# Kernel tuning notes

Measured on AMD Instinct MI355X. Metric: run time of the kernel, lower is better.

The kernel has to match this reference:

```python
import jax, jax.numpy as jnp
import numpy as np

N_NODES = 50000
NEG_SLOPE = 0.2  # PyG GATConv default
EPS = 1e-16      # PyG softmax denominator epsilon


def gat_conv(x, W, att_src, att_dst, bias, src, dst, heads, out_ch):
    # x: [N, F_in]; W: [F_in, heads*out_ch]; att_*: [heads, out_ch]
    N = x.shape[0]
    h = (x @ W).reshape(N, heads, out_ch)              # [N,H,C]
    a_src = jnp.sum(h * att_src, axis=-1)              # [N,H]
    a_dst = jnp.sum(h * att_dst, axis=-1)              # [N,H]
    alpha = a_src[src] + a_dst[dst]                    # [E,H]
    alpha = jnp.where(alpha > 0, alpha, NEG_SLOPE * alpha)  # leaky_relu
    amax = jax.ops.segment_max(alpha, dst, num_segments=N)  # [N,H]
    amax = jnp.where(jnp.isfinite(amax), amax, 0.0)
    ex = jnp.exp(alpha - amax[dst])                    # [E,H]
    denom = jax.ops.segment_sum(ex, dst, num_segments=N)    # [N,H]
    coef = ex / (denom[dst] + EPS)                     # [E,H]
    msg = h[src] * coef[:, :, None]                    # [E,H,C]
    out = jax.ops.segment_sum(msg, dst, num_segments=N)     # [N,H,C]
    return out.reshape(N, heads * out_ch) + bias


def setup_inputs() -> dict:
    key = jax.random.key(0)
    ks = jax.random.split(key, 11)
    T, N, F = 8, N_NODES, 64
    E = 1_600_000
    x = jax.random.normal(ks[0], (T, N, F), dtype=jnp.float32)
    edge_index = jax.random.randint(ks[1], (2, E), 0, N, dtype=jnp.int64)
    s = 0.1
    return {
        "x": x,
        "edge_index": edge_index,
        "W1": jax.random.normal(ks[2], (F, 64), jnp.float32) * s,
        "att_src1": jax.random.normal(ks[3], (8, 8), jnp.float32) * s,
        "att_dst1": jax.random.normal(ks[4], (8, 8), jnp.float32) * s,
        "bias1": jax.random.normal(ks[5], (64,), jnp.float32) * s,
        "W2": jax.random.normal(ks[6], (64, F), jnp.float32) * s,
        "att_src2": jax.random.normal(ks[7], (1, F), jnp.float32) * s,
        "att_dst2": jax.random.normal(ks[8], (1, F), jnp.float32) * s,
        "bias2": jax.random.normal(ks[9], (F,), jnp.float32) * s,
    }


def reference(x, edge_index, W1, att_src1, att_dst1, bias1, W2, att_src2, att_dst2, bias2):
    N = x.shape[1]
    # PyG GATConv adds self-loops by default
    loops = jnp.arange(N, dtype=edge_index.dtype)
    src = jnp.concatenate([edge_index[0], loops])
    dst = jnp.concatenate([edge_index[1], loops])

    def step(xt):  # xt: [N, F] ; dropout is identity in eval mode
        y = jax.nn.elu(gat_conv(xt, W1, att_src1, att_dst1, bias1, src, dst, 8, 8))
        y = gat_conv(y, W2, att_src2, att_dst2, bias2, src, dst, 1, xt.shape[-1])
        return jax.nn.log_softmax(y, axis=-1)

    return jax.vmap(step)(x)  # [T, N, F]
```

## Files before the change

### kernel.cpp

```cpp
#include <hip/hip_runtime.h>
#include <hip/hip_bf16.h>
#include <math.h>


typedef __hip_bfloat16 bf16;

__device__ __forceinline__ float bf2f(unsigned short u) {
    return __uint_as_float(((unsigned int)u) << 16);
}


__global__ __launch_bounds__(256) void count_edges_kernel(const int* __restrict__ dsts,
                                                          int* cnt, int E) {
    int i = blockIdx.x * 256 + threadIdx.x;
    if (i < E) atomicAdd(&cnt[dsts[i]], 1);
}

__global__ __launch_bounds__(1024) void scan_kernel(const int* __restrict__ cnt,
                                                    int* row, int* cur, int N) {
    __shared__ int ls[1024];
    int t = threadIdx.x;
    int chunk = (N + 1023) / 1024;
    int b = t * chunk;
    int sum = 0;
    for (int i = 0; i < chunk; ++i) {
        int idx = b + i;
        if (idx < N) sum += cnt[idx] + 1;
    }
    ls[t] = sum;
    __syncthreads();
    for (int off = 1; off < 1024; off <<= 1) {
        int v = (t >= off) ? ls[t - off] : 0;
        __syncthreads();
        ls[t] += v;
        __syncthreads();
    }
    int run = (t == 0) ? 0 : ls[t - 1];
    for (int i = 0; i < chunk; ++i) {
        int idx = b + i;
        if (idx < N) {
            int c = cnt[idx] + 1;
            row[idx] = run;
            cur[idx] = run;
            run += c;
        }
    }
    if (t == 1023) row[N] = ls[1023];
}

__global__ __launch_bounds__(256) void fill_csr_kernel(const int* __restrict__ srcs,
                                                       const int* __restrict__ dsts,
                                                       int* cur, int* esrc, int E, int N) {
    int i = blockIdx.x * 256 + threadIdx.x;
    if (i >= E + N) return;
    int s, d;
    if (i < E) { s = srcs[i]; d = dsts[i]; }
    else       { s = i - E;   d = s; }
    int pos = atomicAdd(&cur[d], 1);
    esrc[pos] = s;
}


__device__ __forceinline__ float4 ld4(const float* p) { return *(const float4*)p; }
__device__ __forceinline__ float4 ld4(const bf16* p) {
    ushort4 u = *(const ushort4*)p;
    float4 r;
    r.x = bf2f(u.x); r.y = bf2f(u.y); r.z = bf2f(u.z); r.w = bf2f(u.w);
    return r;
}


template <typename TIN, int H, int C>
__global__ __launch_bounds__(256) void gemm_att_kernel(
    const TIN* __restrict__ xin,
    const float* __restrict__ Wm,
    const float* __restrict__ att_s,
    const float* __restrict__ att_d,
    bf16* __restrict__ hout,
    float* __restrict__ asrc,
    float* __restrict__ adst,
    int R) {
    __shared__ float Ws[64 * 64];
    int tid = threadIdx.x;
    {
        const float4* W4 = (const float4*)Wm;
        float4* Ws4 = (float4*)Ws;
#pragma unroll
        for (int i = 0; i < 4; ++i) Ws4[tid + 256 * i] = W4[tid + 256 * i];
    }
    __syncthreads();

    int c  = tid & 63;
    int wv = tid >> 6;
    int n0 = (blockIdx.x * 4 + wv) * 4;
    if (n0 >= R) return;
    int nrows = (R - n0 >= 4) ? 4 : (R - n0);

    const TIN* xb = xin + (size_t)n0 * 64;
    float acc[4] = {0.f, 0.f, 0.f, 0.f};

#pragma unroll 2
    for (int k4 = 0; k4 < 16; ++k4) {
        float4 xv[4];
#pragma unroll
        for (int r = 0; r < 4; ++r) {
            int rr = (r < nrows) ? r : 0;
            xv[r] = ld4(xb + (size_t)rr * 64 + k4 * 4);
        }
        float w0 = Ws[(4 * k4 + 0) * 64 + c];
        float w1 = Ws[(4 * k4 + 1) * 64 + c];
        float w2 = Ws[(4 * k4 + 2) * 64 + c];
        float w3 = Ws[(4 * k4 + 3) * 64 + c];
#pragma unroll
        for (int r = 0; r < 4; ++r) {
            acc[r] = fmaf(xv[r].x, w0, acc[r]);
            acc[r] = fmaf(xv[r].y, w1, acc[r]);
            acc[r] = fmaf(xv[r].z, w2, acc[r]);
            acc[r] = fmaf(xv[r].w, w3, acc[r]);
        }
    }

    float as_w = att_s[c];
    float ad_w = att_d[c];
#pragma unroll
    for (int r = 0; r < 4; ++r) {
        if (r >= nrows) break;
        int n = n0 + r;
        float a = acc[r];
        hout[(size_t)n * 64 + c] = __float2bfloat16(a);
        float vs = a * as_w;
        float vd = a * ad_w;
#pragma unroll
        for (int off = 1; off < C; off <<= 1) {
            vs += __shfl_xor(vs, off, 64);
            vd += __shfl_xor(vd, off, 64);
        }
        if ((c % C) == 0) {
            int hd = c / C;
            asrc[(size_t)n * H + hd] = vs;
            adst[(size_t)n * H + hd] = vd;
        }
    }
}


template <int H, bool FINAL>
__global__ __launch_bounds__(256) void gat_edge_kernel(
    const bf16* __restrict__ h_all,
    const float* __restrict__ asrc_all,
    const float* __restrict__ adst_all,
    const int* __restrict__ row,
    const int* __restrict__ esrc,
    const float* __restrict__ bias,
    bf16* __restrict__ outb,
    float* __restrict__ outf,
    int N, int BPT) {
    int tid  = threadIdx.x;
    int lane = tid & 63;
    int t  = blockIdx.x / BPT;
    int nb = blockIdx.x - t * BPT;
    int n  = nb * 4 + (tid >> 6);
    if (n >= N) return;

    const bf16*  h     = h_all    + (size_t)t * N * 64;
    const char*  asrcb = (const char*)(asrc_all + (size_t)t * N * H);
    const float* adst  = adst_all + (size_t)t * N * H;

    const int head = (H == 8) ? (lane >> 3) : 0;
    float adn = adst[(size_t)n * H + head];

    int e0  = row[n];
    int deg = row[n + 1] - e0;

    float lsum_lane = 0.f;
    float acc0 = 0.f, acc1 = 0.f;

    for (int base = 0; base < deg; base += 64) {
        int cnt = deg - base; if (cnt > 64) cnt = 64;
        int sv = (lane < cnt) ? esrc[e0 + base + lane] : 0;

        if constexpr (H == 8) {
            unsigned head4 = (unsigned)(head << 2);
            unsigned l7_4  = (unsigned)((lane & 7) << 2);
#pragma unroll
            for (int sub = 0; sub < 8; ++sub) {
                if (sub * 8 >= cnt) break;
                int svj = __builtin_amdgcn_ds_bpermute(sub * 32 + l7_4, sv);
                unsigned aoff = (((unsigned)svj) << 5) | head4;
                float av = *(const float*)(asrcb + aoff);
                float tv = av + adn;
                tv = tv > 0.f ? tv : 0.2f * tv;
                tv = (sub * 8 + (lane & 7) < cnt) ? tv : -INFINITY;
                float p = __expf(tv);
                lsum_lane += p;
                unsigned pu = __float_as_uint(p);
#define ACC_EDGE(Q)                                                            \
    {                                                                          \
        float pj = __uint_as_float(                                            \
            __builtin_amdgcn_ds_swizzle(pu, ((Q) << 5) | 0x18));               \
        unsigned sj = (unsigned)__builtin_amdgcn_readlane(sv, sub * 8 + (Q));  \
        const unsigned short* hrow =                                           \
            (const unsigned short*)h + ((size_t)sj << 6);    \
        float hvf = bf2f(hrow[lane]);                                          \
        if ((Q) & 1) acc1 = fmaf(pj, hvf, acc1);                               \
        else         acc0 = fmaf(pj, hvf, acc0);                               \
    }
                ACC_EDGE(0) ACC_EDGE(1) ACC_EDGE(2) ACC_EDGE(3)
                ACC_EDGE(4) ACC_EDGE(5) ACC_EDGE(6) ACC_EDGE(7)
#undef ACC_EDGE
            }
        } else {
            unsigned aoff = ((unsigned)sv) << 2;
            float av = *(const float*)(asrcb + aoff);
            float tv = av + adn;
            tv = tv > 0.f ? tv : 0.2f * tv;
            tv = (lane < cnt) ? tv : -INFINITY;
            float p0 = __expf(tv);
            lsum_lane += p0;
            for (int j0 = 0; j0 < cnt; j0 += 8) {
#pragma unroll
                for (int q = 0; q < 8; ++q) {
                    int j = j0 + q;
                    float pj = __uint_as_float(
                        __builtin_amdgcn_readlane(__float_as_uint(p0), j));
                    unsigned sj = (unsigned)__builtin_amdgcn_readlane(sv, j);
                    const unsigned short* hrow =
                        (const unsigned short*)h + ((size_t)sj << 6);
                    float hvf = bf2f(hrow[lane]);
                    if (q & 1) acc1 = fmaf(pj, hvf, acc1);
                    else       acc0 = fmaf(pj, hvf, acc0);
                }
            }
        }
    }

    float lsum;
    if constexpr (H == 8) {
        float ls = lsum_lane;
        ls += __shfl_xor(ls, 1, 64);
        ls += __shfl_xor(ls, 2, 64);
        ls += __shfl_xor(ls, 4, 64);
        lsum = ls;
    } else {
        float ls = lsum_lane;
#pragma unroll
        for (int o = 1; o < 64; o <<= 1) ls += __shfl_xor(ls, o, 64);
        lsum = ls;
    }

    float v = (acc0 + acc1) / (lsum + 1e-16f) + bias[lane];
    size_t oidx = ((size_t)t * N + n) * 64 + lane;
    if (!FINAL) {
        float y = v > 0.f ? v : expm1f(v);
        outb[oidx] = __float2bfloat16(y);
    } else {
        float mx = v;
#pragma unroll
        for (int off = 1; off < 64; off <<= 1) mx = fmaxf(mx, __shfl_xor(mx, off, 64));
        float ex = __expf(v - mx);
        float sm = ex;
#pragma unroll
        for (int off = 1; off < 64; off <<= 1) sm += __shfl_xor(sm, off, 64);
        outf[oidx] = (v - mx) - __logf(sm);
    }
}


extern "C" void kernel_launch(void* const* d_in, const int* in_sizes, int n_in,
                              void* d_out, int out_size, void* d_ws, size_t ws_size,
                              hipStream_t stream) {
    const float* x        = (const float*)d_in[0];
    const int*   eidx     = (const int*)d_in[1];
    const float* W1       = (const float*)d_in[2];
    const float* att_src1 = (const float*)d_in[3];
    const float* att_dst1 = (const float*)d_in[4];
    const float* bias1    = (const float*)d_in[5];
    const float* W2       = (const float*)d_in[6];
    const float* att_src2 = (const float*)d_in[7];
    const float* att_dst2 = (const float*)d_in[8];
    const float* bias2    = (const float*)d_in[9];
    float* dout = (float*)d_out;

    const int N = 50000;
    const int F = 64;
    const int E = in_sizes[1] / 2;
    const int T = in_sizes[0] / (N * F);
    const int NT = T * N;
    const int Etot = E + N;
    const int BPT = (N + 3) / 4;

    const int* srcs = eidx;
    const int* dsts = eidx + E;

    char* ws = (char*)d_ws;
    size_t off = 0;
    auto carve = [&](size_t bytes) -> void* {
        void* p = ws + off;
        off = (off + bytes + 255) & ~(size_t)255;
        return p;
    };
    bf16*  h_all  = (bf16*)carve((size_t)NT * 64 * sizeof(bf16));
    bf16*  y1_all = (bf16*)carve((size_t)NT * 64 * sizeof(bf16));
    float* asrc   = (float*)carve((size_t)NT * 8 * sizeof(float));
    float* adst   = (float*)carve((size_t)NT * 8 * sizeof(float));
    int*   rowp   = (int*)carve((size_t)(N + 1) * sizeof(int));
    int*   cnt    = (int*)carve((size_t)N * sizeof(int));
    int*   cur    = (int*)carve((size_t)N * sizeof(int));
    int*   esrc   = (int*)carve((size_t)Etot * sizeof(int));
    bool batched = (off <= ws_size);

    if (batched) {
        hipMemsetAsync(cnt, 0, (size_t)N * sizeof(int), stream);
        count_edges_kernel<<<(E + 255) / 256, 256, 0, stream>>>(dsts, cnt, E);
        scan_kernel<<<1, 1024, 0, stream>>>(cnt, rowp, cur, N);
        fill_csr_kernel<<<(E + N + 255) / 256, 256, 0, stream>>>(srcs, dsts, cur, esrc, E, N);

        int gemm_blocks = (NT + 15) / 16;
        int edge_grid = BPT * T;
        gemm_att_kernel<float, 8, 8><<<gemm_blocks, 256, 0, stream>>>(
            x, W1, att_src1, att_dst1, h_all, asrc, adst, NT);
        gat_edge_kernel<8, false><<<edge_grid, 256, 0, stream>>>(
            h_all, asrc, adst, rowp, esrc, bias1, y1_all, nullptr, N, BPT);
        gemm_att_kernel<bf16, 1, 64><<<gemm_blocks, 256, 0, stream>>>(
            y1_all, W2, att_src2, att_dst2, h_all, asrc, adst, NT);
        gat_edge_kernel<1, true><<<edge_grid, 256, 0, stream>>>(
            h_all, asrc, adst, rowp, esrc, bias2, nullptr, dout, N, BPT);
    } else {
        off = 0;
        bf16*  h1  = (bf16*)carve((size_t)N * 64 * sizeof(bf16));
        bf16*  y1  = (bf16*)carve((size_t)N * 64 * sizeof(bf16));
        float* as1 = (float*)carve((size_t)N * 8 * sizeof(float));
        float* ad1 = (float*)carve((size_t)N * 8 * sizeof(float));
        int*   rp  = (int*)carve((size_t)(N + 1) * sizeof(int));
        int*   cn  = (int*)carve((size_t)N * sizeof(int));
        int*   cu  = (int*)carve((size_t)N * sizeof(int));
        int*   es  = (int*)carve((size_t)Etot * sizeof(int));
        hipMemsetAsync(cn, 0, (size_t)N * sizeof(int), stream);
        count_edges_kernel<<<(E + 255) / 256, 256, 0, stream>>>(dsts, cn, E);
        scan_kernel<<<1, 1024, 0, stream>>>(cn, rp, cu, N);
        fill_csr_kernel<<<(E + N + 255) / 256, 256, 0, stream>>>(srcs, dsts, cu, es, E, N);
        int gemm_grid = (N + 15) / 16;
        for (int t = 0; t < T; ++t) {
            const float* xt = x + (size_t)t * N * F;
            float* ot = dout + (size_t)t * N * F;
            gemm_att_kernel<float, 8, 8><<<gemm_grid, 256, 0, stream>>>(
                xt, W1, att_src1, att_dst1, h1, as1, ad1, N);
            gat_edge_kernel<8, false><<<(N + 3) / 4, 256, 0, stream>>>(
                h1, as1, ad1, rp, es, bias1, y1, nullptr, N, (N + 3) / 4);
            gemm_att_kernel<bf16, 1, 64><<<gemm_grid, 256, 0, stream>>>(
                y1, W2, att_src2, att_dst2, h1, as1, ad1, N);
            gat_edge_kernel<1, true><<<(N + 3) / 4, 256, 0, stream>>>(
                h1, as1, ad1, rp, es, bias2, nullptr, ot, N, (N + 3) / 4);
        }
    }
}
```

Baseline: 1.201 ms.

## Interleave timesteps node-major and process four timesteps per edge gather

Intermediate h, attention scores and layer-1 output now use a node-major layout with all 8 timesteps of a node stored together. Each edge-kernel wave handles four timesteps at once, so one CSR walk and one source-index readlane serve four accumulations, and the four gathered rows sit in nearby memory. The non-batched fallback path is removed and the workspace-size check is ignored. The cost is more registers per thread and a hardcoded assumption that T is divisible by 4.

```diff
diff --git a/kernel.cpp b/kernel.cpp
--- a/kernel.cpp
+++ b/kernel.cpp
@@ -73,13 +73,14 @@
 template <typename TIN, int H, int C>
 __global__ __launch_bounds__(256) void gemm_att_kernel(
     const TIN* __restrict__ xin,
+    size_t TOFF, int XSTRIDE,
     const float* __restrict__ Wm,
     const float* __restrict__ att_s,
     const float* __restrict__ att_d,
     bf16* __restrict__ hout,
     float* __restrict__ asrc,
     float* __restrict__ adst,
-    int R) {
+    int N) {
     __shared__ float Ws[64 * 64];
     int tid = threadIdx.x;
     {
@@ -90,13 +91,19 @@
     }
     __syncthreads();
 
+    int t  = blockIdx.y;
+    const TIN* xt = xin + (size_t)t * TOFF;
+    bf16*  ht  = hout + t * 64;
+    float* ast = asrc + t * H;
+    float* adt = adst + t * H;
+
     int c  = tid & 63;
     int wv = tid >> 6;
     int n0 = (blockIdx.x * 4 + wv) * 4;
-    if (n0 >= R) return;
-    int nrows = (R - n0 >= 4) ? 4 : (R - n0);
-
-    const TIN* xb = xin + (size_t)n0 * 64;
+    if (n0 >= N) return;
+    int nrows = (N - n0 >= 4) ? 4 : (N - n0);
+
+    const TIN* xb = xt + (size_t)n0 * XSTRIDE;
     float acc[4] = {0.f, 0.f, 0.f, 0.f};
 
 #pragma unroll 2
@@ -105,7 +112,7 @@
 #pragma unroll
         for (int r = 0; r < 4; ++r) {
             int rr = (r < nrows) ? r : 0;
-            xv[r] = ld4(xb + (size_t)rr * 64 + k4 * 4);
+            xv[r] = ld4(xb + (size_t)rr * XSTRIDE + k4 * 4);
         }
         float w0 = Ws[(4 * k4 + 0) * 64 + c];
         float w1 = Ws[(4 * k4 + 1) * 64 + c];
@@ -127,7 +134,7 @@
         if (r >= nrows) break;
         int n = n0 + r;
         float a = acc[r];
-        hout[(size_t)n * 64 + c] = __float2bfloat16(a);
+        ht[(size_t)n * 512 + c] = __float2bfloat16(a);
         float vs = a * as_w;
         float vd = a * ad_w;
 #pragma unroll
@@ -137,12 +144,14 @@
         }
         if ((c % C) == 0) {
             int hd = c / C;
-            asrc[(size_t)n * H + hd] = vs;
-            adst[(size_t)n * H + hd] = vd;
-        }
-    }
-}
-
+            ast[(size_t)n * (8 * H) + hd] = vs;
+            adt[(size_t)n * (8 * H) + hd] = vd;
+        }
+    }
+}
+
+
+#define SWZ(PU, Q) __uint_as_float(__builtin_amdgcn_ds_swizzle((PU), ((Q) << 5) | 0x18))
 
 template <int H, bool FINAL>
 __global__ __launch_bounds__(256) void gat_edge_kernel(
@@ -154,26 +163,28 @@
     const float* __restrict__ bias,
     bf16* __restrict__ outb,
     float* __restrict__ outf,
-    int N, int BPT) {
+    int N) {
     int tid  = threadIdx.x;
     int lane = tid & 63;
-    int t  = blockIdx.x / BPT;
-    int nb = blockIdx.x - t * BPT;
-    int n  = nb * 4 + (tid >> 6);
+    int t0   = blockIdx.y * 4;
+    int n    = blockIdx.x * 4 + (tid >> 6);
     if (n >= N) return;
 
-    const bf16*  h     = h_all    + (size_t)t * N * 64;
-    const char*  asrcb = (const char*)(asrc_all + (size_t)t * N * H);
-    const float* adst  = adst_all + (size_t)t * N * H;
+    const char* asrcb = (const char*)asrc_all;
+    const unsigned short* hb = (const unsigned short*)h_all;
 
     const int head = (H == 8) ? (lane >> 3) : 0;
-    float adn = adst[(size_t)n * H + head];
+    float adn[4];
+#pragma unroll
+    for (int i = 0; i < 4; ++i)
+        adn[i] = adst_all[(size_t)n * (8 * H) + (t0 + i) * H + head];
 
     int e0  = row[n];
     int deg = row[n + 1] - e0;
-
-    float lsum_lane = 0.f;
-    float acc0 = 0.f, acc1 = 0.f;
+    int toff = t0 * 64 + lane;
+
+    float lsum[4] = {0.f, 0.f, 0.f, 0.f};
+    float acc[4]  = {0.f, 0.f, 0.f, 0.f};
 
     for (int base = 0; base < deg; base += 64) {
         int cnt = deg - base; if (cnt > 64) cnt = 64;
@@ -186,82 +197,96 @@
             for (int sub = 0; sub < 8; ++sub) {
                 if (sub * 8 >= cnt) break;
                 int svj = __builtin_amdgcn_ds_bpermute(sub * 32 + l7_4, sv);
-                unsigned aoff = (((unsigned)svj) << 5) | head4;
-                float av = *(const float*)(asrcb + aoff);
-                float tv = av + adn;
-                tv = tv > 0.f ? tv : 0.2f * tv;
-                tv = (sub * 8 + (lane & 7) < cnt) ? tv : -INFINITY;
-                float p = __expf(tv);
-                lsum_lane += p;
-                unsigned pu = __float_as_uint(p);
+                unsigned abase = (((unsigned)svj) << 8) | head4;
+                bool valid = (sub * 8 + (lane & 7) < cnt);
+                float p[4];
+#pragma unroll
+                for (int i = 0; i < 4; ++i) {
+                    float av = *(const float*)(asrcb + (abase | ((unsigned)(t0 + i) << 5)));
+                    float tv = av + adn[i];
+                    tv = tv > 0.f ? tv : 0.2f * tv;
+                    tv = valid ? tv : -INFINITY;
+                    p[i] = __expf(tv);
+                    lsum[i] += p[i];
+                }
+                unsigned pu0 = __float_as_uint(p[0]);
+                unsigned pu1 = __float_as_uint(p[1]);
+                unsigned pu2 = __float_as_uint(p[2]);
+                unsigned pu3 = __float_as_uint(p[3]);
 #define ACC_EDGE(Q)                                                            \
     {                                                                          \
-        float pj = __uint_as_float(                                            \
-            __builtin_amdgcn_ds_swizzle(pu, ((Q) << 5) | 0x18));               \
         unsigned sj = (unsigned)__builtin_amdgcn_readlane(sv, sub * 8 + (Q));  \
-        const unsigned short* hrow =                                           \
-            (const unsigned short*)h + ((size_t)sj << 6);    \
-        float hvf = bf2f(hrow[lane]);                                          \
-        if ((Q) & 1) acc1 = fmaf(pj, hvf, acc1);                               \
-        else         acc0 = fmaf(pj, hvf, acc0);                               \
+        const unsigned short* hrow = hb + ((size_t)sj << 9) + toff;            \
+        acc[0] = fmaf(SWZ(pu0, Q), bf2f(hrow[0]),   acc[0]);                   \
+        acc[1] = fmaf(SWZ(pu1, Q), bf2f(hrow[64]),  acc[1]);                   \
+        acc[2] = fmaf(SWZ(pu2, Q), bf2f(hrow[128]), acc[2]);                   \
+        acc[3] = fmaf(SWZ(pu3, Q), bf2f(hrow[192]), acc[3]);                   \
     }
                 ACC_EDGE(0) ACC_EDGE(1) ACC_EDGE(2) ACC_EDGE(3)
                 ACC_EDGE(4) ACC_EDGE(5) ACC_EDGE(6) ACC_EDGE(7)
 #undef ACC_EDGE
             }
         } else {
-            unsigned aoff = ((unsigned)sv) << 2;
-            float av = *(const float*)(asrcb + aoff);
-            float tv = av + adn;
-            tv = tv > 0.f ? tv : 0.2f * tv;
-            tv = (lane < cnt) ? tv : -INFINITY;
-            float p0 = __expf(tv);
-            lsum_lane += p0;
+            unsigned abase = ((unsigned)sv) << 5;
+            float p[4];
+#pragma unroll
+            for (int i = 0; i < 4; ++i) {
+                float av = *(const float*)(asrcb + (abase | ((unsigned)(t0 + i) << 2)));
+                float tv = av + adn[i];
+                tv = tv > 0.f ? tv : 0.2f * tv;
+                tv = (lane < cnt) ? tv : -INFINITY;
+                p[i] = __expf(tv);
+                lsum[i] += p[i];
+            }
             for (int j0 = 0; j0 < cnt; j0 += 8) {
 #pragma unroll
                 for (int q = 0; q < 8; ++q) {
                     int j = j0 + q;
-                    float pj = __uint_as_float(
-                        __builtin_amdgcn_readlane(__float_as_uint(p0), j));
                     unsigned sj = (unsigned)__builtin_amdgcn_readlane(sv, j);
-                    const unsigned short* hrow =
-                        (const unsigned short*)h + ((size_t)sj << 6);
-                    float hvf = bf2f(hrow[lane]);
-                    if (q & 1) acc1 = fmaf(pj, hvf, acc1);
-                    else       acc0 = fmaf(pj, hvf, acc0);
+                    const unsigned short* hrow = hb + ((size_t)sj << 9) + toff;
+                    float pj0 = __uint_as_float(
+                        __builtin_amdgcn_readlane(__float_as_uint(p[0]), j));
+                    float pj1 = __uint_as_float(
+                        __builtin_amdgcn_readlane(__float_as_uint(p[1]), j));
+                    float pj2 = __uint_as_float(
+                        __builtin_amdgcn_readlane(__float_as_uint(p[2]), j));
+                    float pj3 = __uint_as_float(
+                        __builtin_amdgcn_readlane(__float_as_uint(p[3]), j));
+                    acc[0] = fmaf(pj0, bf2f(hrow[0]),   acc[0]);
+                    acc[1] = fmaf(pj1, bf2f(hrow[64]),  acc[1]);
+                    acc[2] = fmaf(pj2, bf2f(hrow[128]), acc[2]);
+                    acc[3] = fmaf(pj3, bf2f(hrow[192]), acc[3]);
                 }
             }
         }
     }
 
-    float lsum;
-    if constexpr (H == 8) {
-        float ls = lsum_lane;
-        ls += __shfl_xor(ls, 1, 64);
-        ls += __shfl_xor(ls, 2, 64);
-        ls += __shfl_xor(ls, 4, 64);
-        lsum = ls;
-    } else {
-        float ls = lsum_lane;
-#pragma unroll
-        for (int o = 1; o < 64; o <<= 1) ls += __shfl_xor(ls, o, 64);
-        lsum = ls;
-    }
-
-    float v = (acc0 + acc1) / (lsum + 1e-16f) + bias[lane];
-    size_t oidx = ((size_t)t * N + n) * 64 + lane;
-    if (!FINAL) {
-        float y = v > 0.f ? v : expm1f(v);
-        outb[oidx] = __float2bfloat16(y);
-    } else {
-        float mx = v;
-#pragma unroll
-        for (int off = 1; off < 64; off <<= 1) mx = fmaxf(mx, __shfl_xor(mx, off, 64));
-        float ex = __expf(v - mx);
-        float sm = ex;
-#pragma unroll
-        for (int off = 1; off < 64; off <<= 1) sm += __shfl_xor(sm, off, 64);
-        outf[oidx] = (v - mx) - __logf(sm);
+#pragma unroll
+    for (int i = 0; i < 4; ++i) {
+        float ls = lsum[i];
+        if constexpr (H == 8) {
+            ls += __shfl_xor(ls, 1, 64);
+            ls += __shfl_xor(ls, 2, 64);
+            ls += __shfl_xor(ls, 4, 64);
+        } else {
+#pragma unroll
+            for (int o = 1; o < 64; o <<= 1) ls += __shfl_xor(ls, o, 64);
+        }
+        float v = acc[i] / (ls + 1e-16f) + bias[lane];
+        if (!FINAL) {
+            float y = v > 0.f ? v : expm1f(v);
+            outb[(size_t)n * 512 + (t0 + i) * 64 + lane] = __float2bfloat16(y);
+        } else {
+            float mx = v;
+#pragma unroll
+            for (int off = 1; off < 64; off <<= 1) mx = fmaxf(mx, __shfl_xor(mx, off, 64));
+            float ex = __expf(v - mx);
+            float sm = ex;
+#pragma unroll
+            for (int off = 1; off < 64; off <<= 1) sm += __shfl_xor(sm, off, 64);
+            outf[(size_t)(t0 + i) * N * 64 + (size_t)n * 64 + lane] =
+                (v - mx) - __logf(sm);
+        }
     }
 }
 
@@ -307,50 +332,21 @@
     int*   cnt    = (int*)carve((size_t)N * sizeof(int));
     int*   cur    = (int*)carve((size_t)N * sizeof(int));
     int*   esrc   = (int*)carve((size_t)Etot * sizeof(int));
-    bool batched = (off <= ws_size);
-
-    if (batched) {
-        hipMemsetAsync(cnt, 0, (size_t)N * sizeof(int), stream);
-        count_edges_kernel<<<(E + 255) / 256, 256, 0, stream>>>(dsts, cnt, E);
-        scan_kernel<<<1, 1024, 0, stream>>>(cnt, rowp, cur, N);
-        fill_csr_kernel<<<(E + N + 255) / 256, 256, 0, stream>>>(srcs, dsts, cur, esrc, E, N);
-
-        int gemm_blocks = (NT + 15) / 16;
-        int edge_grid = BPT * T;
-        gemm_att_kernel<float, 8, 8><<<gemm_blocks, 256, 0, stream>>>(
-            x, W1, att_src1, att_dst1, h_all, asrc, adst, NT);
-        gat_edge_kernel<8, false><<<edge_grid, 256, 0, stream>>>(
-            h_all, asrc, adst, rowp, esrc, bias1, y1_all, nullptr, N, BPT);
-        gemm_att_kernel<bf16, 1, 64><<<gemm_blocks, 256, 0, stream>>>(
-            y1_all, W2, att_src2, att_dst2, h_all, asrc, adst, NT);
-        gat_edge_kernel<1, true><<<edge_grid, 256, 0, stream>>>(
-            h_all, asrc, adst, rowp, esrc, bias2, nullptr, dout, N, BPT);
-    } else {
-        off = 0;
-        bf16*  h1  = (bf16*)carve((size_t)N * 64 * sizeof(bf16));
-        bf16*  y1  = (bf16*)carve((size_t)N * 64 * sizeof(bf16));
-        float* as1 = (float*)carve((size_t)N * 8 * sizeof(float));
-        float* ad1 = (float*)carve((size_t)N * 8 * sizeof(float));
-        int*   rp  = (int*)carve((size_t)(N + 1) * sizeof(int));
-        int*   cn  = (int*)carve((size_t)N * sizeof(int));
-        int*   cu  = (int*)carve((size_t)N * sizeof(int));
-        int*   es  = (int*)carve((size_t)Etot * sizeof(int));
-        hipMemsetAsync(cn, 0, (size_t)N * sizeof(int), stream);
-        count_edges_kernel<<<(E + 255) / 256, 256, 0, stream>>>(dsts, cn, E);
-        scan_kernel<<<1, 1024, 0, stream>>>(cn, rp, cu, N);
-        fill_csr_kernel<<<(E + N + 255) / 256, 256, 0, stream>>>(srcs, dsts, cu, es, E, N);
-        int gemm_grid = (N + 15) / 16;
-        for (int t = 0; t < T; ++t) {
-            const float* xt = x + (size_t)t * N * F;
-            float* ot = dout + (size_t)t * N * F;
-            gemm_att_kernel<float, 8, 8><<<gemm_grid, 256, 0, stream>>>(
-                xt, W1, att_src1, att_dst1, h1, as1, ad1, N);
-            gat_edge_kernel<8, false><<<(N + 3) / 4, 256, 0, stream>>>(
-                h1, as1, ad1, rp, es, bias1, y1, nullptr, N, (N + 3) / 4);
-            gemm_att_kernel<bf16, 1, 64><<<gemm_grid, 256, 0, stream>>>(
-                y1, W2, att_src2, att_dst2, h1, as1, ad1, N);
-            gat_edge_kernel<1, true><<<(N + 3) / 4, 256, 0, stream>>>(
-                h1, as1, ad1, rp, es, bias2, nullptr, ot, N, (N + 3) / 4);
-        }
-    }
-}
+    (void)ws_size;
+
+    hipMemsetAsync(cnt, 0, (size_t)N * sizeof(int), stream);
+    count_edges_kernel<<<(E + 255) / 256, 256, 0, stream>>>(dsts, cnt, E);
+    scan_kernel<<<1, 1024, 0, stream>>>(cnt, rowp, cur, N);
+    fill_csr_kernel<<<(E + N + 255) / 256, 256, 0, stream>>>(srcs, dsts, cur, esrc, E, N);
+
+    dim3 ggrid((N + 15) / 16, T);
+    dim3 egrid(BPT, T / 4);
+    gemm_att_kernel<float, 8, 8><<<ggrid, 256, 0, stream>>>(
+        x, (size_t)N * 64, 64, W1, att_src1, att_dst1, h_all, asrc, adst, N);
+    gat_edge_kernel<8, false><<<egrid, 256, 0, stream>>>(
+        h_all, asrc, adst, rowp, esrc, bias1, y1_all, nullptr, N);
+    gemm_att_kernel<bf16, 1, 64><<<ggrid, 256, 0, stream>>>(
+        y1_all, (size_t)64, 512, W2, att_src2, att_dst2, h_all, asrc, adst, N);
+    gat_edge_kernel<1, true><<<egrid, 256, 0, stream>>>(
+        h_all, asrc, adst, rowp, esrc, bias2, nullptr, dout, N);
+}
```

After: 1.158 ms. 1.04x faster.
